# Kernel tuning notes

Hardware: AMD Instinct MI355X
Metric: run time of the kernel (lower is better)

Reference implementation:

```python
import jax, jax.numpy as jnp
import numpy as np
import math

# Derived from BilateralDenoiser.set_influence(1.0):
#   sigma = max(2*influence, 1e-4) = 2.0; window N = 2*ceil(2.5*sigma)+1 = 11
SIGMA = 2.0
NORMAL_POWER = 128.0  # normal-similarity exponent in the CUDA kernel
EPS = 1e-4


def setup_inputs() -> dict:
    key = jax.random.key(0)
    k1, k2, k3 = jax.random.split(key, 3)
    B, H, W = 4, 1024, 1024
    col = jax.random.uniform(k1, (B, H, W, 3), jnp.float32)
    nrm = jax.random.normal(k2, (B, H, W, 3), jnp.float32)
    nrm = nrm / jnp.linalg.norm(nrm, axis=-1, keepdims=True)  # unit normals
    zdz = jax.random.uniform(k3, (B, H, W, 2), jnp.float32)   # (depth, |d depth|)
    return {"col": col, "nrm": nrm, "zdz": zdz}


def _denoise(col, nrm, zdz):
    # col/nrm: [B,H,W,3]; zdz: [B,H,W,2]
    B, H, W, _ = col.shape
    variance = SIGMA * SIGMA
    rad = int(math.ceil(SIGMA * 2.5))  # 5 -> 11x11 window
    yy = jnp.arange(H)
    xx = jnp.arange(W)
    c_z = zdz[..., 0]   # center depth
    c_dz = zdz[..., 1]  # center depth-gradient magnitude
    accum_c = jnp.zeros((B, H, W, 3), col.dtype)
    accum_w = jnp.zeros((B, H, W), col.dtype)
    for dy in range(-rad, rad + 1):
        my = (yy + dy >= 0) & (yy + dy < H)
        for dx in range(-rad, rad + 1):
            mx = (xx + dx >= 0) & (xx + dx < W)
            valid = (my[:, None] & mx[None, :]).astype(col.dtype)  # skip OOB taps
            # tap value at pixel (y+dy, x+dx), vectorized over the whole image
            t_col = jnp.roll(col, (-dy, -dx), axis=(1, 2))
            t_nrm = jnp.roll(nrm, (-dy, -dx), axis=(1, 2))
            t_z = jnp.roll(c_z, (-dy, -dx), axis=(1, 2))
            dist_sqr = float(dx * dx + dy * dy)
            dist = math.sqrt(dist_sqr)
            w_xy = math.exp(-dist_sqr / (2.0 * variance))  # spatial Gaussian (scalar)
            w_n = jnp.clip(jnp.sum(t_nrm * nrm, axis=-1), 0.0, 1.0) ** NORMAL_POWER
            w_d = jnp.exp(-jnp.abs(t_z - c_z) / jnp.maximum(c_dz * dist, EPS))
            w = w_xy * w_n * w_d * valid  # [B,H,W]
            accum_c = accum_c + t_col * w[..., None]
            accum_w = accum_w + w
    # module forward: col_w[..., 0:3] / col_w[..., 3:4]
    return accum_c / accum_w[..., None]


def reference(col, nrm, zdz):
    return _denoise(col, nrm, zdz)
```

## Files before the change

kernel.cpp:

```cpp
#include <hip/hip_runtime.h>

#define RAD 5
#define BX 64
#define BY 16
#define PX 2
#define NTX 32
#define NTY 16
#define NT 512
#define TW (BX + 2*RAD)
#define TH (BY + 2*RAD)
#define HALF (TW/2)
#define NU (2*RAD + PX)

#define LOG2E 1.44269504f
#define CLAMP2 14426.950f
#define PC1 184.664963f
#define PC2 -92.3324814f
#define PC3 61.5549876f

__device__ __constant__ const float kLG[6] = {
    0.0f, -0.18033688f, -0.72134752f, -1.62303192f, -2.88539008f, -4.50842200f};
__device__ __constant__ const float kINVD[6][6] = {
    {1e30f,       1.0f,        0.5f,        0.33333333f, 0.25f,       0.2f},
    {1.0f,        0.70710678f, 0.44721360f, 0.31622777f, 0.24253563f, 0.19611614f},
    {0.5f,        0.44721360f, 0.35355339f, 0.27735010f, 0.22360680f, 0.18569534f},
    {0.33333333f, 0.31622777f, 0.27735010f, 0.23570226f, 0.2f,        0.17149859f},
    {0.25f,       0.24253563f, 0.22360680f, 0.2f,        0.17677670f, 0.15617376f},
    {0.2f,        0.19611614f, 0.18569534f, 0.17149859f, 0.15617376f, 0.14142136f}};

__global__ __launch_bounds__(512, 4) void bilateral_kernel(
    const float* __restrict__ col, const float* __restrict__ nrm,
    const float* __restrict__ zdz, float* __restrict__ out,
    int H, int W) {
  __shared__ float4 s_w[TH][TW];
  __shared__ uint2  s_c[TH][TW];

  const int bx = blockIdx.x, by = blockIdx.y, bz = blockIdx.z;
  const int gx0 = bx * BX - RAD;
  const int gy0 = by * BY - RAD;
  const int tid = threadIdx.x;
  const int plane = bz * H * W;

  for (int i = tid; i < TH * TW; i += NT) {
    const int r = i / TW;
    const int c = i - r * TW;
    const int pc = (c >> 1) + (c & 1) * HALF;
    const int gy = gy0 + r, gx = gx0 + c;
    float4 wv = make_float4(0.f, 0.f, 0.f, 0.f);
    uint2 cv = make_uint2(0u, 0u);
    if ((unsigned)gy < (unsigned)H && (unsigned)gx < (unsigned)W) {
      const int pix = plane + gy * W + gx;
      const float* np_ = nrm + pix * 3;
      wv.x = np_[0]; wv.y = np_[1]; wv.z = np_[2];
      wv.w = zdz[pix * 2];
      const float* cp = col + pix * 3;
      const unsigned ur = (__float_as_uint(cp[0]) + 0x8000u) >> 16;
      const unsigned ug = (__float_as_uint(cp[1]) + 0x8000u) & 0xffff0000u;
      const unsigned ub = (__float_as_uint(cp[2]) + 0x8000u) & 0xffff0000u;
      cv.x = ur | ug;
      cv.y = ub;
    }
    s_w[r][pc] = wv;
    s_c[r][pc] = cv;
  }
  __syncthreads();

  const int tx = tid & (NTX - 1);
  const int ty = tid >> 5;
  const int ly = ty + RAD;
  const int oy = by * BY + ty;
  const int ox0 = bx * BX + tx * PX;

  float cnx[PX], cny[PX], cnz[PX], czv[PX], rc2[PX];
  float accx[PX], accy[PX], accz[PX], accw[PX];
#pragma unroll
  for (int p = 0; p < PX; ++p) {
    const int c = tx * PX + RAD + p;
    const int pc = (c >> 1) + (c & 1) * HALF;
    const float4 wv = s_w[ly][pc];
    cnx[p] = wv.x; cny[p] = wv.y; cnz[p] = wv.z;
    czv[p] = wv.w;
    const float cdz = zdz[(plane + oy * W + ox0 + p) * 2 + 1];
    rc2[p] = LOG2E / cdz;
    accx[p] = 0.f; accy[p] = 0.f; accz[p] = 0.f; accw[p] = 0.f;
  }

#pragma unroll 1
  for (int dy = -RAD; dy <= RAD; ++dy) {
    const int ady = dy < 0 ? -dy : dy;

    const float4* rowW = &s_w[ly + dy][tx];
    const uint2* rowC = &s_c[ly + dy][tx];
    float4 wvs[NU];
    uint2 cvs[NU];
#pragma unroll
    for (int u = 0; u < NU; ++u) {
      const int off = (u >> 1) + (u & 1) * HALF;
      wvs[u] = rowW[off];
      cvs[u] = rowC[off];
    }

    const float kg_ady = kLG[ady];
    const float* irow = kINVD[ady];
    float sA[6];
    float il2s[6][PX];
#pragma unroll
    for (int j = 0; j < 6; ++j) {
      sA[j] = kLG[j] + kg_ady;
      const float iv = irow[j];
#pragma unroll
      for (int p = 0; p < PX; ++p) il2s[j][p] = fminf(rc2[p] * iv, CLAMP2);
    }

#pragma unroll
    for (int u = 0; u < NU; ++u) {
      const float4 wv = wvs[u];
      const uint2 cv = cvs[u];
      const float tr = __uint_as_float(cv.x << 16);
      const float tg = __uint_as_float(cv.x & 0xffff0000u);
      const float tb = __uint_as_float(cv.y);
#pragma unroll
      for (int p = 0; p < PX; ++p) {
        const int dx = u - RAD - p;
        if (dx < -RAD || dx > RAD) continue;
        const int adx = dx < 0 ? -dx : dx;
        const float d1 = fmaf(wv.x, cnx[p],
                         fmaf(wv.y, cny[p], fmaf(wv.z, cnz[p], -1.0f)));
        const float f = fmaxf(d1, -1.0f);
        const float dz = wv.w - czv[p];
        const float ct = fmaf(-fabsf(dz), il2s[adx][p], sA[adx]);
        const float t1 = fmaf(f, PC3, PC2);
        const float t2 = fmaf(f, t1, PC1);
        const float e = fmaf(f, t2, ct);
        const float w = __builtin_amdgcn_exp2f(e);
        accx[p] = fmaf(tr, w, accx[p]);
        accy[p] = fmaf(tg, w, accy[p]);
        accz[p] = fmaf(tb, w, accz[p]);
        accw[p] += w;
      }
    }
  }

#pragma unroll
  for (int p = 0; p < PX; ++p) {
    const int pix = plane + oy * W + ox0 + p;
    const float inv = 1.0f / accw[p];
    float* op = out + pix * 3;
    op[0] = accx[p] * inv;
    op[1] = accy[p] * inv;
    op[2] = accz[p] * inv;
  }
}

extern "C" void kernel_launch(void* const* d_in, const int* in_sizes, int n_in,
                              void* d_out, int out_size, void* d_ws, size_t ws_size,
                              hipStream_t stream) {
  const float* col = (const float*)d_in[0];
  const float* nrm = (const float*)d_in[1];
  const float* zdz = (const float*)d_in[2];
  float* out = (float*)d_out;
  const int H = 1024, W = 1024;
  const int B = in_sizes[0] / (3 * H * W);
  dim3 grid(W / BX, H / BY, B);
  bilateral_kernel<<<grid, dim3(NT), 0, stream>>>(col, nrm, zdz, out, H, W);
}
```

Baseline: 311.1 us.

## Compute two output rows per thread to reuse shared-memory tap loads vertically

Each thread now produces a 2x2 pixel block instead of 2x1. The block height doubles to 32, and each thread walks 12 tile rows, reusing every loaded row of normals, depth and colour for both output rows. This is meant to cut LDS reads per tap and amortise the per-row weight-table setup. In exchange it doubles accumulator and center registers under a 512-thread launch bound, and adds branching for the first and last rows, so occupancy or spilling could suffer.

```diff
diff --git a/kernel.cpp b/kernel.cpp
--- a/kernel.cpp
+++ b/kernel.cpp
@@ -2,8 +2,9 @@
 
 #define RAD 5
 #define BX 64
-#define BY 16
+#define BY 32
 #define PX 2
+#define PY 2
 #define NTX 32
 #define NTY 16
 #define NT 512
@@ -11,6 +12,7 @@
 #define TH (BY + 2*RAD)
 #define HALF (TW/2)
 #define NU (2*RAD + PX)
+#define NTROW (2*RAD + PY)
 
 #define LOG2E 1.44269504f
 #define CLAMP2 14426.950f
@@ -27,6 +29,40 @@
     {0.33333333f, 0.31622777f, 0.27735010f, 0.23570226f, 0.2f,        0.17149859f},
     {0.25f,       0.24253563f, 0.22360680f, 0.2f,        0.17677670f, 0.15617376f},
     {0.2f,        0.19611614f, 0.18569534f, 0.17149859f, 0.15617376f, 0.14142136f}};
+
+#define TAP(qi, adx, p) do {                                                   \
+    const float d1_ = fmaf(wv.x, cnx[qi][p],                                   \
+                      fmaf(wv.y, cny[qi][p], fmaf(wv.z, cnz[qi][p], -1.0f)));  \
+    const float f_ = fmaxf(d1_, -1.0f);                                        \
+    const float dz_ = wv.w - czv[qi][p];                                       \
+    const float ct_ = fmaf(-fabsf(dz_), il2##qi[adx][p], sA##qi[adx]);         \
+    const float t1_ = fmaf(f_, PC3, PC2);                                      \
+    const float t2_ = fmaf(f_, t1_, PC1);                                      \
+    const float e_ = fmaf(f_, t2_, ct_);                                       \
+    const float w_ = __builtin_amdgcn_exp2f(e_);                               \
+    accx[qi][p] = fmaf(tr, w_, accx[qi][p]);                                   \
+    accy[qi][p] = fmaf(tg, w_, accy[qi][p]);                                   \
+    accz[qi][p] = fmaf(tb, w_, accz[qi][p]);                                   \
+    accw[qi][p] += w_;                                                         \
+  } while (0)
+
+#define ROW_LOOP(Q0, Q1)                                                       \
+  _Pragma("unroll")                                                            \
+  for (int u = 0; u < NU; ++u) {                                               \
+    const float4 wv = wvs[u];                                                  \
+    const uint2 cv = rowC[(u >> 1) + (u & 1) * HALF];                          \
+    const float tr = __uint_as_float(cv.x << 16);                              \
+    const float tg = __uint_as_float(cv.x & 0xffff0000u);                      \
+    const float tb = __uint_as_float(cv.y);                                    \
+    _Pragma("unroll")                                                          \
+    for (int p = 0; p < PX; ++p) {                                             \
+      const int dx = u - RAD - p;                                              \
+      if (dx < -RAD || dx > RAD) continue;                                     \
+      const int adx = dx < 0 ? -dx : dx;                                       \
+      if (Q0) TAP(0, adx, p);                                                  \
+      if (Q1) TAP(1, adx, p);                                                  \
+    }                                                                          \
+  }
 
 __global__ __launch_bounds__(512, 4) void bilateral_kernel(
     const float* __restrict__ col, const float* __restrict__ nrm,
@@ -67,88 +103,82 @@
 
   const int tx = tid & (NTX - 1);
   const int ty = tid >> 5;
-  const int ly = ty + RAD;
-  const int oy = by * BY + ty;
+  const int oy0 = by * BY + ty * PY;
   const int ox0 = bx * BX + tx * PX;
 
-  float cnx[PX], cny[PX], cnz[PX], czv[PX], rc2[PX];
-  float accx[PX], accy[PX], accz[PX], accw[PX];
+  float cnx[PY][PX], cny[PY][PX], cnz[PY][PX], czv[PY][PX], rc2[PY][PX];
+  float accx[PY][PX], accy[PY][PX], accz[PY][PX], accw[PY][PX];
 #pragma unroll
-  for (int p = 0; p < PX; ++p) {
-    const int c = tx * PX + RAD + p;
-    const int pc = (c >> 1) + (c & 1) * HALF;
-    const float4 wv = s_w[ly][pc];
-    cnx[p] = wv.x; cny[p] = wv.y; cnz[p] = wv.z;
-    czv[p] = wv.w;
-    const float cdz = zdz[(plane + oy * W + ox0 + p) * 2 + 1];
-    rc2[p] = LOG2E / cdz;
-    accx[p] = 0.f; accy[p] = 0.f; accz[p] = 0.f; accw[p] = 0.f;
+  for (int q = 0; q < PY; ++q) {
+#pragma unroll
+    for (int p = 0; p < PX; ++p) {
+      const int c = tx * PX + RAD + p;
+      const int pc = (c >> 1) + (c & 1) * HALF;
+      const float4 wv = s_w[ty * PY + RAD + q][pc];
+      cnx[q][p] = wv.x; cny[q][p] = wv.y; cnz[q][p] = wv.z;
+      czv[q][p] = wv.w;
+      const float cdz = zdz[(plane + (oy0 + q) * W + ox0 + p) * 2 + 1];
+      rc2[q][p] = LOG2E / cdz;
+      accx[q][p] = 0.f; accy[q][p] = 0.f; accz[q][p] = 0.f; accw[q][p] = 0.f;
+    }
   }
 
 #pragma unroll 1
-  for (int dy = -RAD; dy <= RAD; ++dy) {
-    const int ady = dy < 0 ? -dy : dy;
+  for (int trow = 0; trow < NTROW; ++trow) {
+    const float4* rowW = &s_w[ty * PY + trow][tx];
+    const uint2* rowC = &s_c[ty * PY + trow][tx];
+    float4 wvs[NU];
+#pragma unroll
+    for (int u = 0; u < NU; ++u) wvs[u] = rowW[(u >> 1) + (u & 1) * HALF];
 
-    const float4* rowW = &s_w[ly + dy][tx];
-    const uint2* rowC = &s_c[ly + dy][tx];
-    float4 wvs[NU];
-    uint2 cvs[NU];
+    float sA0[6], sA1[6], il20[6][PX], il21[6][PX];
+    if (trow <= 2 * RAD) {
+      const int dy = trow - RAD;
+      const int ady = dy < 0 ? -dy : dy;
+      const float kg = kLG[ady];
+      const float* irow = kINVD[ady];
 #pragma unroll
-    for (int u = 0; u < NU; ++u) {
-      const int off = (u >> 1) + (u & 1) * HALF;
-      wvs[u] = rowW[off];
-      cvs[u] = rowC[off];
+      for (int j = 0; j < 6; ++j) {
+        sA0[j] = kLG[j] + kg;
+        const float iv = irow[j];
+        il20[j][0] = fminf(rc2[0][0] * iv, CLAMP2);
+        il20[j][1] = fminf(rc2[0][1] * iv, CLAMP2);
+      }
+    }
+    if (trow >= 1) {
+      const int dy = trow - RAD - 1;
+      const int ady = dy < 0 ? -dy : dy;
+      const float kg = kLG[ady];
+      const float* irow = kINVD[ady];
+#pragma unroll
+      for (int j = 0; j < 6; ++j) {
+        sA1[j] = kLG[j] + kg;
+        const float iv = irow[j];
+        il21[j][0] = fminf(rc2[1][0] * iv, CLAMP2);
+        il21[j][1] = fminf(rc2[1][1] * iv, CLAMP2);
+      }
     }
 
-    const float kg_ady = kLG[ady];
-    const float* irow = kINVD[ady];
-    float sA[6];
-    float il2s[6][PX];
-#pragma unroll
-    for (int j = 0; j < 6; ++j) {
-      sA[j] = kLG[j] + kg_ady;
-      const float iv = irow[j];
-#pragma unroll
-      for (int p = 0; p < PX; ++p) il2s[j][p] = fminf(rc2[p] * iv, CLAMP2);
-    }
-
-#pragma unroll
-    for (int u = 0; u < NU; ++u) {
-      const float4 wv = wvs[u];
-      const uint2 cv = cvs[u];
-      const float tr = __uint_as_float(cv.x << 16);
-      const float tg = __uint_as_float(cv.x & 0xffff0000u);
-      const float tb = __uint_as_float(cv.y);
-#pragma unroll
-      for (int p = 0; p < PX; ++p) {
-        const int dx = u - RAD - p;
-        if (dx < -RAD || dx > RAD) continue;
-        const int adx = dx < 0 ? -dx : dx;
-        const float d1 = fmaf(wv.x, cnx[p],
-                         fmaf(wv.y, cny[p], fmaf(wv.z, cnz[p], -1.0f)));
-        const float f = fmaxf(d1, -1.0f);
-        const float dz = wv.w - czv[p];
-        const float ct = fmaf(-fabsf(dz), il2s[adx][p], sA[adx]);
-        const float t1 = fmaf(f, PC3, PC2);
-        const float t2 = fmaf(f, t1, PC1);
-        const float e = fmaf(f, t2, ct);
-        const float w = __builtin_amdgcn_exp2f(e);
-        accx[p] = fmaf(tr, w, accx[p]);
-        accy[p] = fmaf(tg, w, accy[p]);
-        accz[p] = fmaf(tb, w, accz[p]);
-        accw[p] += w;
-      }
+    if (trow == 0) {
+      ROW_LOOP(1, 0)
+    } else if (trow == NTROW - 1) {
+      ROW_LOOP(0, 1)
+    } else {
+      ROW_LOOP(1, 1)
     }
   }
 
 #pragma unroll
-  for (int p = 0; p < PX; ++p) {
-    const int pix = plane + oy * W + ox0 + p;
-    const float inv = 1.0f / accw[p];
-    float* op = out + pix * 3;
-    op[0] = accx[p] * inv;
-    op[1] = accy[p] * inv;
-    op[2] = accz[p] * inv;
+  for (int q = 0; q < PY; ++q) {
+#pragma unroll
+    for (int p = 0; p < PX; ++p) {
+      const int pix = plane + (oy0 + q) * W + ox0 + p;
+      const float inv = 1.0f / accw[q][p];
+      float* op = out + pix * 3;
+      op[0] = accx[q][p] * inv;
+      op[1] = accy[q][p] * inv;
+      op[2] = accz[q][p] * inv;
+    }
   }
 }
 
```

After: 1.144 ms. 3.68x slower.
